# Kernel tuning notes

Measured on AMD Instinct MI355X. Metric: run time of the kernel, lower is better.

The kernel has to match this reference:

```python
import jax, jax.numpy as jnp
import numpy as np

H = 1024; NH = 16; HD = H // NH  # hidden, heads, head_dim

def setup_inputs() -> dict:
    key = jax.random.key(0)
    ks = jax.random.split(key, 9)
    s = 1.0 / np.sqrt(H)
    return {
        "hidden_states": jax.random.normal(ks[0], (2, 2048, H), jnp.float32),
        "Wq": jax.random.uniform(ks[1], (H, H), jnp.float32, -s, s),
        "bq": jnp.zeros((H,), jnp.float32),
        "Wk": jax.random.uniform(ks[2], (H, H), jnp.float32, -s, s),
        "bk": jnp.zeros((H,), jnp.float32),
        "Wv": jax.random.uniform(ks[3], (H, H), jnp.float32, -s, s),
        "bv": jnp.zeros((H,), jnp.float32),
        "Wo": jax.random.uniform(ks[4], (H, H), jnp.float32, -s, s),
        "bo": jnp.zeros((H,), jnp.float32),
    }

def reference(hidden_states, Wq, bq, Wk, bk, Wv, bv, Wo, bo):
    B, S, _ = hidden_states.shape
    def heads(x):  # [B,S,H] -> [B,NH,S,HD]
        return x.reshape(B, S, NH, HD).transpose(0, 2, 1, 3)
    q = heads(hidden_states @ Wq + bq)
    k = heads(hidden_states @ Wk + bk)
    v = heads(hidden_states @ Wv + bv)
    scores = jnp.einsum('bhqd,bhkd->bhqk', q, k) / jnp.sqrt(jnp.float32(HD))
    causal = jnp.where(jnp.tril(jnp.ones((S, S), bool)), 0.0, -jnp.inf)
    probs = jax.nn.softmax(scores + causal[None, None], axis=-1)
    ctx = jnp.einsum('bhqk,bhkd->bhqd', probs, v)
    ctx = ctx.transpose(0, 2, 1, 3).reshape(B, S, H)
    return ctx @ Wo + bo
```

## Files before the change

### kernel.cpp

```cpp
#include <hip/hip_runtime.h>
#include <hip/hip_bf16.h>

#define BB 2
#define SS 2048
#define HH 1024
#define NHH 16
#define HDD 64
#define MM (BB*SS)
#define QKV_N (3*HH)

typedef _Float16 f16x8 __attribute__((ext_vector_type(8)));
typedef _Float16 f16x4 __attribute__((ext_vector_type(4)));
typedef float f32x4 __attribute__((ext_vector_type(4)));

#define MFMA16(a,b,c)  __builtin_amdgcn_mfma_f32_16x16x32_f16((a),(b),(c),0,0,0)
#define MFMA16K16(a,b,c) __builtin_amdgcn_mfma_f32_16x16x16f16((a),(b),(c),0,0,0)

__device__ __forceinline__ void gl2lds16(const _Float16* g, _Float16* l) {
    __builtin_amdgcn_global_load_lds(
        (const __attribute__((address_space(1))) void*)g,
        (__attribute__((address_space(3))) void*)l, 16, 0, 0);
}

__device__ __forceinline__ float fexp2(float x) { return __builtin_amdgcn_exp2f(x); }

__global__ __launch_bounds__(256) void prep_kernel(
    const float* __restrict__ X,
    const float* __restrict__ W0, const float* __restrict__ W1,
    const float* __restrict__ W2, const float* __restrict__ W3,
    _Float16* __restrict__ Xh,
    _Float16* __restrict__ WqkvT, _Float16* __restrict__ WoT)
{
    __shared__ float t[64][65];
    int z = blockIdx.z;
    int tid = threadIdx.x;
    if (z == 4) {
        int base = (blockIdx.y * 16 + blockIdx.x) * 256 + tid;
        const float4* xin = (const float4*)X;
        f16x4* xout = (f16x4*)Xh;
#pragma unroll
        for (int i = 0; i < 16; ++i) {
            float4 v = xin[base + i * 65536];
            f16x4 hh = {(_Float16)v.x, (_Float16)v.y, (_Float16)v.z, (_Float16)v.w};
            xout[base + i * 65536] = hh;
        }
        return;
    }
    const float* src = (z == 0) ? W0 : (z == 1) ? W1 : (z == 2) ? W2 : W3;
    _Float16* dst = (z < 3) ? (WqkvT + (size_t)z * HH * HH) : WoT;
    int k0 = blockIdx.y * 64, n0 = blockIdx.x * 64;
#pragma unroll
    for (int p = 0; p < 4; ++p) {
        int row = p * 16 + (tid >> 4);
        int col4 = (tid & 15) * 4;
        float4 v = *(const float4*)&src[(size_t)(k0 + row) * HH + n0 + col4];
        t[row][col4 + 0] = v.x; t[row][col4 + 1] = v.y;
        t[row][col4 + 2] = v.z; t[row][col4 + 3] = v.w;
    }
    __syncthreads();
#pragma unroll
    for (int p = 0; p < 2; ++p) {
        int nc = p * 32 + (tid >> 3);
        int ch = tid & 7;
        f16x8 o;
#pragma unroll
        for (int j = 0; j < 8; ++j) o[j] = (_Float16)t[ch * 8 + j][nc];
        *(f16x8*)&dst[(size_t)(n0 + nc) * HH + k0 + ch * 8] = o;
    }
}

template<int MODE>
__global__ __launch_bounds__(256) void gemm128_kernel(
    const _Float16* __restrict__ A, const _Float16* __restrict__ Bt,
    const float* __restrict__ bias0, const float* __restrict__ bias1, const float* __restrict__ bias2,
    _Float16* __restrict__ Qh, _Float16* __restrict__ Kh, _Float16* __restrict__ Vt,
    float* __restrict__ Out)
{
    const int K = HH;
    const int NT = K / 32;
    __shared__ _Float16 smem[24576];

    int row0 = blockIdx.y * 128, n0 = blockIdx.x * 128;
    int tid = threadIdx.x;
    int w = tid >> 6, l = tid & 63, m16 = l & 15, quad = l >> 4;
    int wm = w >> 1, wn = w & 1;

    int srow = w * 32 + (l >> 2);
    int sch = (l & 3) ^ ((l >> 2) & 3) ^ ((l >> 4) & 3);
    const _Float16* aptr = A + (size_t)(row0 + srow) * K + sch * 8;
    const _Float16* bptr = Bt + (size_t)(n0 + srow) * K + sch * 8;

    int gsw = (m16 & 3) ^ ((m16 >> 2) & 3);
    int acol = (quad ^ gsw) * 8;

    f32x4 zero4 = {0.f, 0.f, 0.f, 0.f};
    f32x4 acc[4][4];
#pragma unroll
    for (int i = 0; i < 4; ++i)
#pragma unroll
        for (int j = 0; j < 4; ++j) acc[i][j] = zero4;

    auto stage = [&](int t, int s) {
        int k0 = t * 32;
        int ao = s * 4096 + (w * 32) * 32;
        int bo = 12288 + s * 4096 + (w * 32) * 32;
        gl2lds16(aptr + k0, smem + ao);
        gl2lds16(aptr + (size_t)16 * K + k0, smem + ao + 16 * 32);
        gl2lds16(bptr + k0, smem + bo);
        gl2lds16(bptr + (size_t)16 * K + k0, smem + bo + 16 * 32);
    };

    stage(0, 0);
    stage(1, 1);
    int cur = 0;
    for (int t = 0; t < NT; ++t) {
        if (t < NT - 1) asm volatile("s_waitcnt vmcnt(4)" ::: "memory");
        else            asm volatile("s_waitcnt vmcnt(0)" ::: "memory");
        asm volatile("s_barrier" ::: "memory");
        if (t + 2 < NT) {
            int nxt = cur + 2; if (nxt >= 3) nxt -= 3;
            stage(t + 2, nxt);
        }
        const _Float16* Asr = smem + cur * 4096;
        const _Float16* Bsr = smem + 12288 + cur * 4096;
        f16x8 af[4], bf[4];
#pragma unroll
        for (int i = 0; i < 4; ++i)
            af[i] = *(const f16x8*)&Asr[(wm * 64 + i * 16 + m16) * 32 + acol];
#pragma unroll
        for (int j = 0; j < 4; ++j)
            bf[j] = *(const f16x8*)&Bsr[(wn * 64 + j * 16 + m16) * 32 + acol];
#pragma unroll
        for (int i = 0; i < 4; ++i)
#pragma unroll
            for (int j = 0; j < 4; ++j)
                acc[i][j] = MFMA16(af[i], bf[j], acc[i][j]);
        cur = (cur == 2) ? 0 : cur + 1;
    }

    if (MODE == 1) {
#pragma unroll
        for (int j = 0; j < 4; ++j) {
            int n = n0 + wn * 64 + j * 16 + m16;
            float bi = bias0[n];
#pragma unroll
            for (int i = 0; i < 4; ++i)
#pragma unroll
                for (int r = 0; r < 4; ++r) {
                    int mg = row0 + wm * 64 + i * 16 + quad * 4 + r;
                    Out[(size_t)mg * HH + n] = acc[i][j][r] + bi;
                }
        }
        return;
    }

    int which = n0 >> 10;
    const float* bias = (which == 0) ? bias0 : (which == 1) ? bias1 : bias2;
    __syncthreads();
#pragma unroll
    for (int j = 0; j < 4; ++j) {
        int n_local = wn * 64 + j * 16 + m16;
        float bi = bias[(n0 + n_local) & 1023];
#pragma unroll
        for (int i = 0; i < 4; ++i)
#pragma unroll
            for (int r = 0; r < 4; ++r) {
                int m_local = wm * 64 + i * 16 + quad * 4 + r;
                float v = acc[i][j][r] + bi;
                if (which == 0) v *= 0.18033688011112042f;
                if (which == 2) smem[n_local * 132 + m_local] = (_Float16)v;
                else            smem[m_local * 132 + n_local] = (_Float16)v;
            }
    }
    __syncthreads();

    int b = row0 >> 11, s0 = row0 & 2047;
    if (which == 2) {
#pragma unroll
        for (int p = 0; p < 8; ++p) {
            int n_local = p * 16 + (tid >> 4);
            int schunk = tid & 15;
            f16x8 v = *(const f16x8*)&smem[n_local * 132 + schunk * 8];
            int nw = (n0 + n_local) & 1023;
            int hh = nw >> 6, d = nw & 63;
            *(f16x8*)&Vt[((size_t)(b * NHH + hh) * HDD + d) * SS + s0 + schunk * 8] = v;
        }
    } else {
        _Float16* dst = (which == 0) ? Qh : Kh;
        int hh0 = (n0 & 1023) >> 6;
#pragma unroll
        for (int p = 0; p < 8; ++p) {
            int m_local = p * 16 + (tid >> 4);
            int seg = tid & 15;
            f16x8 v = *(const f16x8*)&smem[m_local * 132 + seg * 8];
            int hh = hh0 + (seg >> 3), d = (seg & 7) * 8;
            *(f16x8*)&dst[((size_t)(b * NHH + hh) * SS + s0 + m_local) * HDD + d] = v;
        }
    }
}

__global__ __launch_bounds__(256, 2) void attn_kernel(
    const _Float16* __restrict__ Qh, const _Float16* __restrict__ Kh,
    const _Float16* __restrict__ Vt, _Float16* __restrict__ Ctx)
{
    __shared__ _Float16 KV[3 * 8192];

    int tid = threadIdx.x;
    int w = tid >> 6, l = tid & 63;
    int m16 = l & 15, quad = l >> 4;
    int b = blockIdx.z, h = blockIdx.y;
    int tA = blockIdx.x, tB = 31 - tA;

    const _Float16* Q = Qh + (size_t)(b * NHH + h) * SS * HDD;
    const _Float16* K = Kh + (size_t)(b * NHH + h) * SS * HDD;
    const _Float16* V = Vt + (size_t)(b * NHH + h) * HDD * SS;

    int qbA = tA * 64 + w * 16, qbB = tB * 64 + w * 16;
    int qA = qbA + m16, qB = qbB + m16;
    f16x8 aqA0 = *(const f16x8*)(Q + (size_t)qA * HDD + quad * 8);
    f16x8 aqA1 = *(const f16x8*)(Q + (size_t)qA * HDD + 32 + quad * 8);
    f16x8 aqB0 = *(const f16x8*)(Q + (size_t)qB * HDD + quad * 8);
    f16x8 aqB1 = *(const f16x8*)(Q + (size_t)qB * HDD + 32 + quad * 8);

    int srow = w * 16 + (l >> 3);
    int sch = (l & 7) ^ (l >> 3);
    const _Float16* kg = K + (size_t)srow * HDD + sch * 8;
    const _Float16* vg = V + (size_t)srow * SS + sch * 8;

    auto stage = [&](int t, int s) {
        int kt = t * 64;
        _Float16* kb = &KV[s * 8192];
        _Float16* vb = &KV[s * 8192 + 4096];
        gl2lds16(kg + (size_t)kt * HDD, kb + (w * 16) * 64);
        gl2lds16(kg + (size_t)(kt + 8) * HDD, kb + (w * 16 + 8) * 64);
        gl2lds16(vg + kt, vb + (w * 16) * 64);
        gl2lds16(vg + (size_t)8 * SS + kt, vb + (w * 16 + 8) * 64);
    };

    int swz = m16 & 7;
    int cka = (quad ^ swz) * 8;
    int ckb = ((quad + 4) ^ swz) * 8;
    int vco[4];
#pragma unroll
    for (int s = 0; s < 4; ++s)
        vco[s] = (((s * 2 + (quad >> 1)) ^ swz) * 8) + (quad & 1) * 4;

    f32x4 zero4 = {0.f, 0.f, 0.f, 0.f};
    const f16x4 ones4 = {(_Float16)1.f, (_Float16)1.f, (_Float16)1.f, (_Float16)1.f};
    f32x4 oA[4], oB[4];
#pragma unroll
    for (int c = 0; c < 4; ++c) { oA[c] = zero4; oB[c] = zero4; }
    f32x4 laccA = zero4, laccB = zero4;

    stage(0, 0);
    if (1 <= tB) stage(1, 1);
    int cur = 0;
    for (int t = 0; t <= tB; ++t) {
        int kt = t * 64;
        if (t < tB) asm volatile("s_waitcnt vmcnt(4)" ::: "memory");
        else        asm volatile("s_waitcnt vmcnt(0)" ::: "memory");
        asm volatile("s_barrier" ::: "memory");
        if (t + 2 <= tB) {
            int nxt = cur + 2; if (nxt >= 3) nxt -= 3;
            stage(t + 2, nxt);
        }

        const _Float16* kb = &KV[cur * 8192];
        const _Float16* vb = &KV[cur * 8192 + 4096];
        f16x8 bk[4][2];
#pragma unroll
        for (int s = 0; s < 4; ++s) {
            const _Float16* kr = kb + (s * 16 + m16) * 64;
            bk[s][0] = *(const f16x8*)(kr + cka);
            bk[s][1] = *(const f16x8*)(kr + ckb);
        }
        f16x4 av[4][4];
#pragma unroll
        for (int c = 0; c < 4; ++c) {
            const _Float16* vr = vb + (c * 16 + m16) * 64;
#pragma unroll
            for (int s = 0; s < 4; ++s)
                av[c][s] = *(const f16x4*)(vr + vco[s]);
        }

        auto body = [&](const f16x8& q0, const f16x8& q1, int qlane,
                        f32x4* o, f32x4& lacc, bool masked) {
            f32x4 st[4];
#pragma unroll
            for (int s = 0; s < 4; ++s) {
                st[s] = MFMA16(bk[s][0], q0, zero4);
                st[s] = MFMA16(bk[s][1], q1, st[s]);
            }
            f16x4 pt[4];
#pragma unroll
            for (int s = 0; s < 4; ++s) {
#pragma unroll
                for (int r = 0; r < 4; ++r) {
                    float p = fexp2(st[s][r]);
                    if (masked) {
                        int key = kt + s * 16 + quad * 4 + r;
                        if (key > qlane) p = 0.f;
                    }
                    pt[s][r] = (_Float16)p;
                }
                lacc = MFMA16K16(ones4, pt[s], lacc);
            }
#pragma unroll
            for (int c = 0; c < 4; ++c)
#pragma unroll
                for (int s = 0; s < 4; ++s)
                    o[c] = MFMA16K16(av[c][s], pt[s], o[c]);
        };

        if (t == tB) body(aqB0, aqB1, qB, oB, laccB, true);
        else         body(aqB0, aqB1, qB, oB, laccB, false);
        if (t == tA)      body(aqA0, aqA1, qA, oA, laccA, true);
        else if (t < tA)  body(aqA0, aqA1, qA, oA, laccA, false);

        cur = (cur == 2) ? 0 : cur + 1;
    }

#pragma unroll
    for (int half = 0; half < 2; ++half) {
        f32x4* o = half ? oB : oA;
        float rs = half ? laccB[0] : laccA[0];
        int qg = half ? qB : qA;
        float inv = 1.0f / rs;
        size_t rowoff = ((size_t)(b * SS) + qg) * HH + h * HDD;
#pragma unroll
        for (int c = 0; c < 4; ++c) {
            f16x4 ov;
#pragma unroll
            for (int r = 0; r < 4; ++r) ov[r] = (_Float16)(o[c][r] * inv);
            *(f16x4*)&Ctx[rowoff + c * 16 + quad * 4] = ov;
        }
    }
}

extern "C" void kernel_launch(void* const* d_in, const int* in_sizes, int n_in,
                              void* d_out, int out_size, void* d_ws, size_t ws_size,
                              hipStream_t stream) {
    const float* hs = (const float*)d_in[0];
    const float* Wq = (const float*)d_in[1];
    const float* bq = (const float*)d_in[2];
    const float* Wk = (const float*)d_in[3];
    const float* bk = (const float*)d_in[4];
    const float* Wv = (const float*)d_in[5];
    const float* bv = (const float*)d_in[6];
    const float* Wo = (const float*)d_in[7];
    const float* bo = (const float*)d_in[8];
    float* out = (float*)d_out;

    size_t off = 0;
    auto alloc = [&](size_t bytes) {
        void* p = (char*)d_ws + off;
        off += (bytes + 255) & ~(size_t)255;
        return p;
    };
    _Float16* Xh    = (_Float16*)alloc((size_t)MM * HH * 2);
    _Float16* WqkvT = (_Float16*)alloc((size_t)3 * HH * HH * 2);
    _Float16* WoT   = (_Float16*)alloc((size_t)HH * HH * 2);
    _Float16* Qh    = (_Float16*)alloc((size_t)BB * NHH * SS * HDD * 2);
    _Float16* Kh    = (_Float16*)alloc((size_t)BB * NHH * SS * HDD * 2);
    _Float16* Vt    = (_Float16*)alloc((size_t)BB * NHH * SS * HDD * 2);
    _Float16* Ctx   = (_Float16*)alloc((size_t)MM * HH * 2);

    prep_kernel<<<dim3(16, 16, 5), 256, 0, stream>>>(
        hs, Wq, Wk, Wv, Wo, Xh, WqkvT, WoT);
    gemm128_kernel<0><<<dim3(QKV_N / 128, MM / 128), 256, 0, stream>>>(
        Xh, WqkvT, bq, bk, bv, Qh, Kh, Vt, nullptr);
    attn_kernel<<<dim3(16, NHH, BB), 256, 0, stream>>>(Qh, Kh, Vt, Ctx);
    gemm128_kernel<1><<<dim3(HH / 128, MM / 128), 256, 0, stream>>>(
        Ctx, WoT, bo, bo, bo, nullptr, nullptr, nullptr, out);
}
```

Baseline: 191.1 us.

## Split attention query tiles across two wave groups in 512-thread blocks

```diff
diff --git a/kernel.cpp b/kernel.cpp
--- a/kernel.cpp
+++ b/kernel.cpp
@@ -199,7 +199,7 @@
     }
 }
 
-__global__ __launch_bounds__(256, 2) void attn_kernel(
+__global__ __launch_bounds__(512, 4) void attn_kernel(
     const _Float16* __restrict__ Qh, const _Float16* __restrict__ Kh,
     const _Float16* __restrict__ Vt, _Float16* __restrict__ Ctx)
 {
@@ -210,19 +210,18 @@
     int m16 = l & 15, quad = l >> 4;
     int b = blockIdx.z, h = blockIdx.y;
     int tA = blockIdx.x, tB = 31 - tA;
+    int half = w >> 2, wq = w & 3;
+    int myT = half ? tB : tA;
 
     const _Float16* Q = Qh + (size_t)(b * NHH + h) * SS * HDD;
     const _Float16* K = Kh + (size_t)(b * NHH + h) * SS * HDD;
     const _Float16* V = Vt + (size_t)(b * NHH + h) * HDD * SS;
 
-    int qbA = tA * 64 + w * 16, qbB = tB * 64 + w * 16;
-    int qA = qbA + m16, qB = qbB + m16;
-    f16x8 aqA0 = *(const f16x8*)(Q + (size_t)qA * HDD + quad * 8);
-    f16x8 aqA1 = *(const f16x8*)(Q + (size_t)qA * HDD + 32 + quad * 8);
-    f16x8 aqB0 = *(const f16x8*)(Q + (size_t)qB * HDD + quad * 8);
-    f16x8 aqB1 = *(const f16x8*)(Q + (size_t)qB * HDD + 32 + quad * 8);
-
-    int srow = w * 16 + (l >> 3);
+    int q = myT * 64 + wq * 16 + m16;
+    f16x8 aq0 = *(const f16x8*)(Q + (size_t)q * HDD + quad * 8);
+    f16x8 aq1 = *(const f16x8*)(Q + (size_t)q * HDD + 32 + quad * 8);
+
+    int srow = w * 8 + (l >> 3);
     int sch = (l & 7) ^ (l >> 3);
     const _Float16* kg = K + (size_t)srow * HDD + sch * 8;
     const _Float16* vg = V + (size_t)srow * SS + sch * 8;
@@ -231,10 +230,8 @@
         int kt = t * 64;
         _Float16* kb = &KV[s * 8192];
         _Float16* vb = &KV[s * 8192 + 4096];
-        gl2lds16(kg + (size_t)kt * HDD, kb + (w * 16) * 64);
-        gl2lds16(kg + (size_t)(kt + 8) * HDD, kb + (w * 16 + 8) * 64);
-        gl2lds16(vg + kt, vb + (w * 16) * 64);
-        gl2lds16(vg + (size_t)8 * SS + kt, vb + (w * 16 + 8) * 64);
+        gl2lds16(kg + (size_t)kt * HDD, kb + (w * 8) * 64);
+        gl2lds16(vg + kt, vb + (w * 8) * 64);
     };
 
     int swz = m16 & 7;
@@ -247,17 +244,17 @@
 
     f32x4 zero4 = {0.f, 0.f, 0.f, 0.f};
     const f16x4 ones4 = {(_Float16)1.f, (_Float16)1.f, (_Float16)1.f, (_Float16)1.f};
-    f32x4 oA[4], oB[4];
-#pragma unroll
-    for (int c = 0; c < 4; ++c) { oA[c] = zero4; oB[c] = zero4; }
-    f32x4 laccA = zero4, laccB = zero4;
+    f32x4 o[4];
+#pragma unroll
+    for (int c = 0; c < 4; ++c) o[c] = zero4;
+    f32x4 lacc = zero4;
 
     stage(0, 0);
-    if (1 <= tB) stage(1, 1);
+    stage(1, 1);
     int cur = 0;
     for (int t = 0; t <= tB; ++t) {
         int kt = t * 64;
-        if (t < tB) asm volatile("s_waitcnt vmcnt(4)" ::: "memory");
+        if (t < tB) asm volatile("s_waitcnt vmcnt(2)" ::: "memory");
         else        asm volatile("s_waitcnt vmcnt(0)" ::: "memory");
         asm volatile("s_barrier" ::: "memory");
         if (t + 2 <= tB) {
@@ -265,75 +262,70 @@
             stage(t + 2, nxt);
         }
 
-        const _Float16* kb = &KV[cur * 8192];
-        const _Float16* vb = &KV[cur * 8192 + 4096];
-        f16x8 bk[4][2];
-#pragma unroll
-        for (int s = 0; s < 4; ++s) {
-            const _Float16* kr = kb + (s * 16 + m16) * 64;
-            bk[s][0] = *(const f16x8*)(kr + cka);
-            bk[s][1] = *(const f16x8*)(kr + ckb);
-        }
-        f16x4 av[4][4];
-#pragma unroll
-        for (int c = 0; c < 4; ++c) {
-            const _Float16* vr = vb + (c * 16 + m16) * 64;
+        if (t <= myT) {
+            const _Float16* kb = &KV[cur * 8192];
+            const _Float16* vb = &KV[cur * 8192 + 4096];
+            f16x8 bk[4][2];
+#pragma unroll
+            for (int s = 0; s < 4; ++s) {
+                const _Float16* kr = kb + (s * 16 + m16) * 64;
+                bk[s][0] = *(const f16x8*)(kr + cka);
+                bk[s][1] = *(const f16x8*)(kr + ckb);
+            }
+            f16x4 av[4][4];
+#pragma unroll
+            for (int c = 0; c < 4; ++c) {
+                const _Float16* vr = vb + (c * 16 + m16) * 64;
+#pragma unroll
+                for (int s = 0; s < 4; ++s)
+                    av[c][s] = *(const f16x4*)(vr + vco[s]);
+            }
+
+            f32x4 st[4];
+#pragma unroll
+            for (int s = 0; s < 4; ++s) {
+                st[s] = MFMA16(bk[s][0], aq0, zero4);
+                st[s] = MFMA16(bk[s][1], aq1, st[s]);
+            }
+            f16x4 pt[4];
+            if (t == myT) {
+#pragma unroll
+                for (int s = 0; s < 4; ++s)
+#pragma unroll
+                    for (int r = 0; r < 4; ++r) {
+                        float p = fexp2(st[s][r]);
+                        int key = kt + s * 16 + quad * 4 + r;
+                        if (key > q) p = 0.f;
+                        pt[s][r] = (_Float16)p;
+                    }
+            } else {
+#pragma unroll
+                for (int s = 0; s < 4; ++s)
+#pragma unroll
+                    for (int r = 0; r < 4; ++r)
+                        pt[s][r] = (_Float16)fexp2(st[s][r]);
+            }
 #pragma unroll
             for (int s = 0; s < 4; ++s)
-                av[c][s] = *(const f16x4*)(vr + vco[s]);
-        }
-
-        auto body = [&](const f16x8& q0, const f16x8& q1, int qlane,
-                        f32x4* o, f32x4& lacc, bool masked) {
-            f32x4 st[4];
-#pragma unroll
-            for (int s = 0; s < 4; ++s) {
-                st[s] = MFMA16(bk[s][0], q0, zero4);
-                st[s] = MFMA16(bk[s][1], q1, st[s]);
-            }
-            f16x4 pt[4];
-#pragma unroll
-            for (int s = 0; s < 4; ++s) {
-#pragma unroll
-                for (int r = 0; r < 4; ++r) {
-                    float p = fexp2(st[s][r]);
-                    if (masked) {
-                        int key = kt + s * 16 + quad * 4 + r;
-                        if (key > qlane) p = 0.f;
-                    }
-                    pt[s][r] = (_Float16)p;
-                }
                 lacc = MFMA16K16(ones4, pt[s], lacc);
-            }
 #pragma unroll
             for (int c = 0; c < 4; ++c)
 #pragma unroll
                 for (int s = 0; s < 4; ++s)
                     o[c] = MFMA16K16(av[c][s], pt[s], o[c]);
-        };
-
-        if (t == tB) body(aqB0, aqB1, qB, oB, laccB, true);
-        else         body(aqB0, aqB1, qB, oB, laccB, false);
-        if (t == tA)      body(aqA0, aqA1, qA, oA, laccA, true);
-        else if (t < tA)  body(aqA0, aqA1, qA, oA, laccA, false);
+        }
 
         cur = (cur == 2) ? 0 : cur + 1;
     }
 
-#pragma unroll
-    for (int half = 0; half < 2; ++half) {
-        f32x4* o = half ? oB : oA;
-        float rs = half ? laccB[0] : laccA[0];
-        int qg = half ? qB : qA;
-        float inv = 1.0f / rs;
-        size_t rowoff = ((size_t)(b * SS) + qg) * HH + h * HDD;
-#pragma unroll
-        for (int c = 0; c < 4; ++c) {
-            f16x4 ov;
-#pragma unroll
-            for (int r = 0; r < 4; ++r) ov[r] = (_Float16)(o[c][r] * inv);
-            *(f16x4*)&Ctx[rowoff + c * 16 + quad * 4] = ov;
-        }
+    float inv = 1.0f / lacc[0];
+    size_t rowoff = ((size_t)(b * SS) + q) * HH + h * HDD;
+#pragma unroll
+    for (int c = 0; c < 4; ++c) {
+        f16x4 ov;
+#pragma unroll
+        for (int r = 0; r < 4; ++r) ov[r] = (_Float16)(o[c][r] * inv);
+        *(f16x4*)&Ctx[rowoff + c * 16 + quad * 4] = ov;
     }
 }
 
@@ -369,7 +361,7 @@
         hs, Wq, Wk, Wv, Wo, Xh, WqkvT, WoT);
     gemm128_kernel<0><<<dim3(QKV_N / 128, MM / 128), 256, 0, stream>>>(
         Xh, WqkvT, bq, bk, bv, Qh, Kh, Vt, nullptr);
-    attn_kernel<<<dim3(16, NHH, BB), 256, 0, stream>>>(Qh, Kh, Vt, Ctx);
+    attn_kernel<<<dim3(16, NHH, BB), 512, 0, stream>>>(Qh, Kh, Vt, Ctx);
     gemm128_kernel<1><<<dim3(HH / 128, MM / 128), 256, 0, stream>>>(
         Ctx, WoT, bo, bo, bo, nullptr, nullptr, nullptr, out);
 }
```

Result: faster. 181.2 us (-5.2%).
